# Kernel optimization log

Measured on AMD Instinct MI355X. Metric: run time of the kernel, lower is better.

## Reference

```python
import jax, jax.numpy as jnp
import numpy as np

N = 200000
NNZ = 6400000
E = 500000
IN_P, IN_F, IN_N = 62, 37, 37
HID, LAT, DEC_HID = 256, 128, 64


def _p(key, shape, scale=0.05):
    return scale * jax.random.normal(key, shape, dtype=jnp.float32)


def setup_inputs() -> dict:
    key = jax.random.key(0)
    ks = jax.random.split(key, 32)
    inp = {
        'x_process': jax.random.normal(ks[0], (N, IN_P), dtype=jnp.float32),
        'x_file': jax.random.normal(ks[1], (N, IN_F), dtype=jnp.float32),
        'x_network': jax.random.normal(ks[2], (N, IN_N), dtype=jnp.float32),
        'adj_rows': jax.random.randint(ks[3], (NNZ,), 0, N, dtype=jnp.int32),
        'adj_cols': jax.random.randint(ks[4], (NNZ,), 0, N, dtype=jnp.int32),
        'adj_vals': jax.random.uniform(ks[5], (NNZ,), dtype=jnp.float32) / 32.0,
        'edge_src': jax.random.randint(ks[6], (E,), 0, N, dtype=jnp.int32),
        'edge_dst': jax.random.randint(ks[7], (E,), 0, N, dtype=jnp.int32),
        # per-view encoder params (weights stored [in, out])
        'Wp1': _p(ks[8], (IN_P, HID)), 'bp1': jnp.zeros((HID,), jnp.float32),
        'Wp2': _p(ks[9], (HID, LAT)), 'bp2': jnp.zeros((LAT,), jnp.float32),
        'Wf1': _p(ks[10], (IN_F, HID)), 'bf1': jnp.zeros((HID,), jnp.float32),
        'Wf2': _p(ks[11], (HID, LAT)), 'bf2': jnp.zeros((LAT,), jnp.float32),
        'Wn1': _p(ks[12], (IN_N, HID)), 'bn1': jnp.zeros((HID,), jnp.float32),
        'Wn2': _p(ks[13], (HID, LAT)), 'bn2': jnp.zeros((LAT,), jnp.float32),
        # gates
        'Wgp': _p(ks[14], (LAT, 1)), 'bgp': jnp.zeros((1,), jnp.float32),
        'Wgf': _p(ks[15], (LAT, 1)), 'bgf': jnp.zeros((1,), jnp.float32),
        'Wgn': _p(ks[16], (LAT, 1)), 'bgn': jnp.zeros((1,), jnp.float32),
        # mlp edge decoder
        'Wd1': _p(ks[17], (4 * LAT, DEC_HID)), 'bd1': jnp.zeros((DEC_HID,), jnp.float32),
        'Wd2': _p(ks[18], (DEC_HID, 1)), 'bd2': jnp.zeros((1,), jnp.float32),
    }
    return inp


def _spmm(rows, cols, vals, x):
    # sparse (COO) adjacency @ dense x : gather cols, scale, scatter-add into rows
    return jax.ops.segment_sum(vals[:, None] * x[cols], rows, num_segments=N)


def _encode_view(x, rows, cols, vals, W1, b1, W2, b2):
    h = jax.nn.relu(_spmm(rows, cols, vals, x) @ W1 + b1)  # dropout=0 / eval mode
    return _spmm(rows, cols, vals, h) @ W2 + b2


def reference(x_process, x_file, x_network, adj_rows, adj_cols, adj_vals,
              edge_src, edge_dst,
              Wp1, bp1, Wp2, bp2, Wf1, bf1, Wf2, bf2, Wn1, bn1, Wn2, bn2,
              Wgp, bgp, Wgf, bgf, Wgn, bgn, Wd1, bd1, Wd2, bd2):
    zp = _encode_view(x_process, adj_rows, adj_cols, adj_vals, Wp1, bp1, Wp2, bp2)
    zf = _encode_view(x_file, adj_rows, adj_cols, adj_vals, Wf1, bf1, Wf2, bf2)
    zn = _encode_view(x_network, adj_rows, adj_cols, adj_vals, Wn1, bn1, Wn2, bn2)
    # multi-view softmax gating -> fused latent [N, LAT]
    scores = jnp.concatenate([zp @ Wgp + bgp, zf @ Wgf + bgf, zn @ Wgn + bgn], axis=1)
    alpha = jax.nn.softmax(scores, axis=1)
    z = alpha[:, 0:1] * zp + alpha[:, 1:2] * zf + alpha[:, 2:3] * zn
    # mlp edge decoder: gather src/dst, concat features, small MLP
    zs, zd = z[edge_src], z[edge_dst]
    feats = jnp.concatenate([zs, zd, zs * zd, jnp.abs(zs - zd)], axis=1)  # [E, 4*LAT]
    logits = jax.nn.relu(feats @ Wd1 + bd1) @ Wd2 + bd2
    return logits[:, 0]
```

## Files before the change

kernel.cpp:

```cpp
#include <hip/hip_runtime.h>
#include <math.h>

#define Nn 200000
#define NNZV 6400000
#define NE 500000
#define HID 256
#define LAT 128

typedef _Float16 h2 __attribute__((ext_vector_type(2)));
typedef _Float16 f16x4 __attribute__((ext_vector_type(4)));
typedef _Float16 f16x8 __attribute__((ext_vector_type(8)));
typedef float f32x4 __attribute__((ext_vector_type(4)));
typedef short s16x8 __attribute__((ext_vector_type(8)));
struct alignas(8) H4 { _Float16 h[4]; };

__global__ __launch_bounds__(256) void k_zero(int* __restrict__ cnt){
  int i = blockIdx.x*256 + threadIdx.x;
  if(i < Nn) cnt[i] = 0;
}

__global__ __launch_bounds__(256) void k_count(const int* __restrict__ rows, int* __restrict__ cnt){
  int i = blockIdx.x*256 + threadIdx.x;
  if(i < NNZV) atomicAdd(&cnt[rows[i]], 1);
}

__global__ __launch_bounds__(512) void k_scan_block(const int* __restrict__ cnt, int* __restrict__ incl, int* __restrict__ bsum){
  __shared__ int s[512];
  int t = threadIdx.x;
  int i = blockIdx.x*512 + t;
  int v = (i < Nn) ? cnt[i] : 0;
  s[t] = v; __syncthreads();
  for(int off = 1; off < 512; off <<= 1){
    int x = (t >= off) ? s[t-off] : 0;
    __syncthreads();
    s[t] += x;
    __syncthreads();
  }
  if(i < Nn) incl[i] = s[t];
  if(t == 511) bsum[blockIdx.x] = s[t];
}

__global__ __launch_bounds__(512) void k_scan_bsum(int* __restrict__ bsum, int nb){
  __shared__ int s[512];
  int t = threadIdx.x;
  int v = (t < nb) ? bsum[t] : 0;
  s[t] = v; __syncthreads();
  for(int off = 1; off < 512; off <<= 1){
    int x = (t >= off) ? s[t-off] : 0;
    __syncthreads();
    s[t] += x;
    __syncthreads();
  }
  if(t < nb) bsum[t] = s[t] - v;
}

__global__ __launch_bounds__(256) void k_finish(const int* __restrict__ incl, const int* __restrict__ boff,
                                                int* __restrict__ row_ptr, int* __restrict__ cur){
  int i = blockIdx.x*256 + threadIdx.x;
  if(i < Nn){
    int v = incl[i] + boff[i >> 9];
    row_ptr[i+1] = v;
    if(i < Nn-1) cur[i+1] = v;
  }
  if(i == 0){ row_ptr[0] = 0; cur[0] = 0; }
}

__global__ __launch_bounds__(256) void k_scatter(const int* __restrict__ rows, const int* __restrict__ cols,
    const float* __restrict__ vals, int* __restrict__ cur,
    int* __restrict__ cols_s, _Float16* __restrict__ vals_s){
  int i = blockIdx.x*256 + threadIdx.x;
  if(i >= NNZV) return;
  int r = rows[i];
  int j = atomicAdd(&cur[r], 1);
  cols_s[j] = cols[i];
  vals_s[j] = (_Float16)vals[i];
}

__global__ __launch_bounds__(256) void k_xpack(const float* __restrict__ xp, const float* __restrict__ xf,
    const float* __restrict__ xn, _Float16* __restrict__ xc0, _Float16* __restrict__ xtl){
  int idx = blockIdx.x*256 + threadIdx.x;
  int row = idx/18, c8 = idx - row*18;
  if(row >= Nn) return;
  H4 ha, hb;
  #pragma unroll
  for(int q = 0; q < 8; q++){
    int c = c8*8 + q;
    float x;
    if(c < 62)       x = xp[row*62 + c];
    else if(c < 99)  x = xf[row*37 + (c-62)];
    else if(c == 99) x = 0.f;
    else if(c < 137) x = xn[row*37 + (c-100)];
    else             x = 0.f;
    if(q < 4) ha.h[q] = (_Float16)x; else hb.h[q-4] = (_Float16)x;
  }
  if(c8 < 16){
    *(H4*)&xc0[(size_t)row*128 + c8*8]     = ha;
    *(H4*)&xc0[(size_t)row*128 + c8*8 + 4] = hb;
  } else {
    int t = (c8-16)*8;
    *(H4*)&xtl[(size_t)row*16 + t]     = ha;
    *(H4*)&xtl[(size_t)row*16 + t + 4] = hb;
  }
}

__global__ __launch_bounds__(256) void k_wpackF(
    const float* __restrict__ Wp1, const float* __restrict__ Wf1, const float* __restrict__ Wn1,
    const float* __restrict__ Wp2, const float* __restrict__ Wf2, const float* __restrict__ Wn2,
    const float* __restrict__ Wd1,
    _Float16* __restrict__ w1fp, _Float16* __restrict__ w1ff, _Float16* __restrict__ w1fn,
    _Float16* __restrict__ w2fp, _Float16* __restrict__ w2ff, _Float16* __restrict__ w2fn,
    _Float16* __restrict__ wdf){
  int i = blockIdx.x*256 + threadIdx.x;
  if(i >= 22528) return;
  f16x8 o;
  if(i >= 18432){
    int r = i - 18432;
    int w = r >> 10, kt = (r >> 8) & 3, nt = (r >> 6) & 3, l = r & 63;
    int krow = w*128 + kt*32 + (l>>4)*8, col = nt*16 + (l&15);
    #pragma unroll
    for(int j = 0; j < 8; j++)
      o[j] = (_Float16)Wd1[(krow + j)*64 + col];
    *(f16x8*)&wdf[(size_t)r*8] = o;
    return;
  }
  int v = i / 6144, rem = i - v*6144;
  const float* W1 = (v==0)?Wp1:((v==1)?Wf1:Wn1);
  const float* W2 = (v==0)?Wp2:((v==1)?Wf2:Wn2);
  _Float16* d1 = (v==0)?w1fp:((v==1)?w1ff:w1fn);
  _Float16* d2 = (v==0)?w2fp:((v==1)?w2ff:w2fn);
  int Kv = (v==0)?62:37;
  if(rem < 2048){
    int kt = rem >> 10, r2 = rem & 1023;
    int nt = r2 >> 6, l = r2 & 63;
    int krow = kt*32 + (l>>4)*8, col = nt*16 + (l&15);
    #pragma unroll
    for(int j = 0; j < 8; j++){
      int k = krow + j;
      o[j] = (k < Kv) ? (_Float16)W1[k*256 + col] : (_Float16)0.f;
    }
    *(f16x8*)&d1[rem*8] = o;
  } else {
    int r = rem - 2048;
    int kt = r >> 9, nt = (r >> 6) & 7, l = r & 63;
    int krow = kt*32 + (l>>4)*8, col = nt*16 + (l&15);
    #pragma unroll
    for(int j = 0; j < 8; j++)
      o[j] = (_Float16)W2[(krow + j)*128 + col];
    *(f16x8*)&d2[r*8] = o;
  }
}

__global__ void k_const(const float* b2p, const float* Wgp, const float* bgp,
                        const float* b2f, const float* Wgf, const float* bgf,
                        const float* b2n, const float* Wgn, const float* bgn,
                        float* c3){
  int l = threadIdx.x;
  float p = 0.f, f = 0.f, n = 0.f;
  for(int j = l; j < LAT; j += 64){
    p += b2p[j]*Wgp[j];
    f += b2f[j]*Wgf[j];
    n += b2n[j]*Wgn[j];
  }
  #pragma unroll
  for(int off = 32; off >= 1; off >>= 1){
    p += __shfl_xor(p, off);
    f += __shfl_xor(f, off);
    n += __shfl_xor(n, off);
  }
  if(l == 0){ c3[0] = p + bgp[0]; c3[1] = f + bgf[0]; c3[2] = n + bgn[0]; }
}

__device__ __forceinline__ void encode_view(
    int tid, int row0, int voff, int Kv, int vidx,
    const _Float16 (*sT)[152], _Float16 (*sTv)[72], _Float16 (*hT)[264],
    const _Float16* __restrict__ w1frag, const float* __restrict__ b1,
    const _Float16* __restrict__ w2frag,
    _Float16* __restrict__ Y3){
  int w = tid >> 6, l = tid & 63;
  int kg = l >> 4, er = l & 15;
  int mrow = (w & 1)*16 + er;

  {
    int row = tid >> 3, c0 = (tid & 7)*8;
    f16x8 vv;
    #pragma unroll
    for(int q = 0; q < 8; q++){
      int c = c0 + q;
      vv[q] = (c < Kv) ? sT[row][voff + c] : (_Float16)0.f;
    }
    *(f16x8*)&sTv[row][c0] = vv;
  }
  __syncthreads();

  {
    f16x8 a0 = *(const f16x8*)&sTv[mrow][kg*8];
    f16x8 a1 = *(const f16x8*)&sTv[mrow][32 + kg*8];
    int ntb = (w >> 1)*8;
    #pragma unroll
    for(int nt8 = 0; nt8 < 8; nt8++){
      int nt = ntb + nt8;
      f16x8 b0 = *(const f16x8*)&w1frag[(size_t)((0*16 + nt)*64 + l)*8];
      f16x8 b1v = *(const f16x8*)&w1frag[(size_t)((1*16 + nt)*64 + l)*8];
      f32x4 acc = {0.f, 0.f, 0.f, 0.f};
      acc = __builtin_amdgcn_mfma_f32_16x16x32_f16(a0, b0, acc, 0, 0, 0);
      acc = __builtin_amdgcn_mfma_f32_16x16x32_f16(a1, b1v, acc, 0, 0, 0);
      int col = nt*16 + er;
      float bb = b1[col];
      #pragma unroll
      for(int j = 0; j < 4; j++)
        hT[(w & 1)*16 + kg*4 + j][col] = (_Float16)fmaxf(acc[j] + bb, 0.f);
    }
  }
  __syncthreads();

  {
    f16x8 af[8];
    #pragma unroll
    for(int kt = 0; kt < 8; kt++)
      af[kt] = *(const f16x8*)&hT[mrow][kt*32 + kg*8];
    __syncthreads();
    _Float16* yst = &hT[0][0];
    int ntb = (w >> 1)*4;
    #pragma unroll
    for(int nt4 = 0; nt4 < 4; nt4++){
      int nt = ntb + nt4;
      f32x4 acc = {0.f, 0.f, 0.f, 0.f};
      #pragma unroll
      for(int kt = 0; kt < 8; kt++){
        f16x8 bf = *(const f16x8*)&w2frag[(size_t)((kt*8 + nt)*64 + l)*8];
        acc = __builtin_amdgcn_mfma_f32_16x16x32_f16(af[kt], bf, acc, 0, 0, 0);
      }
      int col = nt*16 + er;
      #pragma unroll
      for(int j = 0; j < 4; j++)
        yst[((w & 1)*16 + kg*4 + j)*132 + col] = (_Float16)acc[j];
    }
    __syncthreads();
    int row = tid >> 3, c0 = (tid & 7)*16;
    f16x8 y0 = *(const f16x8*)&yst[row*132 + c0];
    f16x8 y1 = *(const f16x8*)&yst[row*132 + c0 + 8];
    _Float16* yo = &Y3[(size_t)(row0 + row)*384 + vidx*128 + c0];
    *(f16x8*)yo       = y0;
    *(f16x8*)(yo + 8) = y1;
  }
  __syncthreads();
}

__global__ __launch_bounds__(256, 5) void k_encfused(
    const int* __restrict__ row_ptr, const int* __restrict__ cols_s, const _Float16* __restrict__ vals_s,
    const _Float16* __restrict__ xc0, const _Float16* __restrict__ xtl,
    const _Float16* __restrict__ w1fp, const float* __restrict__ bp1, const _Float16* __restrict__ w2fp,
    const _Float16* __restrict__ w1ff, const float* __restrict__ bf1, const _Float16* __restrict__ w2ff,
    const _Float16* __restrict__ w1fn, const float* __restrict__ bn1, const _Float16* __restrict__ w2fn,
    _Float16* __restrict__ Y3){
  __shared__ _Float16 sT[32][152];
  __shared__ _Float16 sTv[32][72];
  __shared__ _Float16 hT[32][264];
  int tid = threadIdx.x;
  int lane = tid & 63, wid = tid >> 6;
  int hl = lane & 31;
  int half = lane >> 5;
  int base = lane & 32;
  int row0 = blockIdx.x * 32;
  bool hast = (hl < 4);
  const char* xc0b = (const char*)xc0;
  const char* xtlb = (const char*)xtl;

  for(int p = 0; p < 4; p++){
    int rr = wid*8 + p*2 + half;
    int r = row0 + rr;
    int start = row_ptr[r], end = row_ptr[r+1];
    int len = end - start;
    int lenO = __shfl(len, lane ^ 32);
    int lenmax = len > lenO ? len : lenO;
    float a0 = 0.f, a1 = 0.f, a2 = 0.f, a3 = 0.f;
    float t0 = 0.f, t1 = 0.f, t2 = 0.f, t3 = 0.f;
    for(int j0 = 0; j0 < lenmax; j0 += 32){
      int m = len - j0; if(m > 32) m = 32; if(m < 0) m = 0;
      int mO = lenO - j0; if(mO > 32) mO = 32; if(mO < 0) mO = 0;
      int mmax = m > mO ? m : mO;
      int mycol = 0; float myval = 0.f;
      if(hl < m){
        mycol = cols_s[start + j0 + hl];
        myval = (float)vals_s[start + j0 + hl];
      }
      int mpad = (mmax + 3) & ~3;
      for(int k = 0; k < mpad; k += 4){
        #pragma unroll
        for(int q = 0; q < 4; q++){
          int c = __shfl(mycol, base + k + q);
          float v = __shfl(myval, base + k + q);
          f16x4 xa = *(const f16x4*)(xc0b + (((unsigned)c) << 8) + hl*8);
          a0 = fmaf((float)xa[0], v, a0);
          a1 = fmaf((float)xa[1], v, a1);
          a2 = fmaf((float)xa[2], v, a2);
          a3 = fmaf((float)xa[3], v, a3);
          if(hast){
            f16x4 xb = *(const f16x4*)(xtlb + ((unsigned)c)*32u + hl*8);
            t0 = fmaf((float)xb[0], v, t0);
            t1 = fmaf((float)xb[1], v, t1);
            t2 = fmaf((float)xb[2], v, t2);
            t3 = fmaf((float)xb[3], v, t3);
          }
        }
      }
    }
    h2 s01; s01[0] = (_Float16)a0; s01[1] = (_Float16)a1;
    h2 s23; s23[0] = (_Float16)a2; s23[1] = (_Float16)a3;
    *(h2*)&sT[rr][4*hl]     = s01;
    *(h2*)&sT[rr][4*hl + 2] = s23;
    if(hast){
      h2 u01; u01[0] = (_Float16)t0; u01[1] = (_Float16)t1;
      h2 u23; u23[0] = (_Float16)t2; u23[1] = (_Float16)t3;
      *(h2*)&sT[rr][128 + 4*hl]     = u01;
      *(h2*)&sT[rr][128 + 4*hl + 2] = u23;
    }
  }
  __syncthreads();

  encode_view(tid, row0, 0,   62, 0, sT, sTv, hT, w1fp, bp1, w2fp, Y3);
  encode_view(tid, row0, 62,  37, 1, sT, sTv, hT, w1ff, bf1, w2ff, Y3);
  encode_view(tid, row0, 100, 37, 2, sT, sTv, hT, w1fn, bn1, w2fn, Y3);
}

__global__ __launch_bounds__(256, 8) void k_spmm2f(
    const int* __restrict__ row_ptr, const int* __restrict__ cols_s, const _Float16* __restrict__ vals_s,
    const _Float16* __restrict__ Y3,
    const float* __restrict__ Wgp, const float* __restrict__ Wgf, const float* __restrict__ Wgn,
    const float* __restrict__ c3,
    const float* __restrict__ b2p, const float* __restrict__ b2f, const float* __restrict__ b2n,
    _Float16* __restrict__ z){
  int tid = threadIdx.x;
  int lane = tid & 63;
  int hl = lane & 31;
  int half = lane >> 5;
  int base = lane & 32;
  int r = blockIdx.x*8 + (tid >> 6)*2 + half;
  int start = row_ptr[r], end = row_ptr[r+1];
  int len = end - start;
  int lenO = __shfl(len, lane ^ 32);
  int lenmax = len > lenO ? len : lenO;
  unsigned lo = hl*8;
  float ap0=0.f, ap1=0.f, ap2=0.f, ap3=0.f;
  float af0=0.f, af1=0.f, af2=0.f, af3=0.f;
  float an0=0.f, an1=0.f, an2=0.f, an3=0.f;
  const char* Yb = (const char*)Y3;
  for(int j0 = 0; j0 < lenmax; j0 += 32){
    int m = len - j0; if(m > 32) m = 32; if(m < 0) m = 0;
    int mO = lenO - j0; if(mO > 32) mO = 32; if(mO < 0) mO = 0;
    int mmax = m > mO ? m : mO;
    int mycol = 0; float myval = 0.f;
    if(hl < m){
      mycol = cols_s[start + j0 + hl];
      myval = (float)vals_s[start + j0 + hl];
    }
    int mpad = (mmax + 3) & ~3;
    for(int k = 0; k < mpad; k += 4){
      #pragma unroll
      for(int q = 0; q < 4; q++){
        int c = __shfl(mycol, base + k + q);
        float v = __shfl(myval, base + k + q);
        const char* p = Yb + ((unsigned)c)*768u + lo;
        f16x4 yp = *(const f16x4*)(p);
        f16x4 yf = *(const f16x4*)(p + 256);
        f16x4 yn = *(const f16x4*)(p + 512);
        ap0 = fmaf((float)yp[0], v, ap0); ap1 = fmaf((float)yp[1], v, ap1);
        ap2 = fmaf((float)yp[2], v, ap2); ap3 = fmaf((float)yp[3], v, ap3);
        af0 = fmaf((float)yf[0], v, af0); af1 = fmaf((float)yf[1], v, af1);
        af2 = fmaf((float)yf[2], v, af2); af3 = fmaf((float)yf[3], v, af3);
        an0 = fmaf((float)yn[0], v, an0); an1 = fmaf((float)yn[1], v, an1);
        an2 = fmaf((float)yn[2], v, an2); an3 = fmaf((float)yn[3], v, an3);
      }
    }
  }
  int o = hl*4;
  float4 wp = *(const float4*)&Wgp[o];
  float4 wf = *(const float4*)&Wgf[o];
  float4 wn = *(const float4*)&Wgn[o];
  float scp = ap0*wp.x + ap1*wp.y + ap2*wp.z + ap3*wp.w;
  float scf = af0*wf.x + af1*wf.y + af2*wf.z + af3*wf.w;
  float scn = an0*wn.x + an1*wn.y + an2*wn.z + an3*wn.w;
  #pragma unroll
  for(int off = 16; off >= 1; off >>= 1){
    scp += __shfl_xor(scp, off);
    scf += __shfl_xor(scf, off);
    scn += __shfl_xor(scn, off);
  }
  float sp = scp + c3[0], sf = scf + c3[1], sn = scn + c3[2];
  float mx = fmaxf(sp, fmaxf(sf, sn));
  float ep = expf(sp - mx), ef = expf(sf - mx), en = expf(sn - mx);
  float inv = 1.f / (ep + ef + en);
  float A0 = ep*inv, A1 = ef*inv, A2 = en*inv;
  float4 bp = *(const float4*)&b2p[o];
  float4 bf = *(const float4*)&b2f[o];
  float4 bn = *(const float4*)&b2n[o];
  H4 uz;
  uz.h[0] = (_Float16)(A0*(ap0 + bp.x) + A1*(af0 + bf.x) + A2*(an0 + bn.x));
  uz.h[1] = (_Float16)(A0*(ap1 + bp.y) + A1*(af1 + bf.y) + A2*(an1 + bn.y));
  uz.h[2] = (_Float16)(A0*(ap2 + bp.z) + A1*(af2 + bf.z) + A2*(an2 + bn.z));
  uz.h[3] = (_Float16)(A0*(ap3 + bp.w) + A1*(af3 + bf.w) + A2*(an3 + bn.w));
  *(H4*)&z[(size_t)r*LAT + o] = uz;
}

#define DEC_TILES (NE/16)
__global__ __launch_bounds__(256) void k_dec(
    const _Float16* __restrict__ z, const int* __restrict__ esrc, const int* __restrict__ edst,
    const _Float16* __restrict__ wdf, const float* __restrict__ bd1,
    const float* __restrict__ Wd2, const float* __restrict__ bd2, float* __restrict__ out){
  __shared__ float part[4][16][68];
  int tid = threadIdx.x;
  int w  = tid >> 6;
  int l  = tid & 63;
  int erow = l & 15;
  int kg   = l >> 4;
  const f16x8* wb = (const f16x8*)wdf + (size_t)w*1024 + l;

  int n0 = (tid & 15) * 4;
  int e2 = tid >> 4;
  float4 bb1 = *(const float4*)&bd1[n0];
  float4 w2v = *(const float4*)&Wd2[n0];
  float bias2 = bd2[0];

  for(int tile = blockIdx.x; tile < DEC_TILES; tile += gridDim.x){
    int e = tile*16 + erow;
    int si = esrc[e], di = edst[e];
    const f16x8* zs = (const f16x8*)&z[(size_t)si*LAT];
    const f16x8* zd = (const f16x8*)&z[(size_t)di*LAT];
    f16x8 afr[4];
    if(w == 0){
      #pragma unroll
      for(int kt = 0; kt < 4; kt++) afr[kt] = zs[kt*4 + kg];
    } else if(w == 1){
      #pragma unroll
      for(int kt = 0; kt < 4; kt++) afr[kt] = zd[kt*4 + kg];
    } else if(w == 2){
      #pragma unroll
      for(int kt = 0; kt < 4; kt++) afr[kt] = zs[kt*4 + kg] * zd[kt*4 + kg];
    } else {
      #pragma unroll
      for(int kt = 0; kt < 4; kt++){
        f16x8 d = zs[kt*4 + kg] - zd[kt*4 + kg];
        s16x8 m = __builtin_bit_cast(s16x8, d) & (short)0x7fff;
        afr[kt] = __builtin_bit_cast(f16x8, m);
      }
    }
    f32x4 zero = {0.f, 0.f, 0.f, 0.f};
    f32x4 acc[4] = {zero, zero, zero, zero};
    #pragma unroll
    for(int kt = 0; kt < 4; kt++){
      #pragma unroll
      for(int nt = 0; nt < 4; nt++){
        f16x8 bf = wb[kt*256 + nt*64];
        acc[nt] = __builtin_amdgcn_mfma_f32_16x16x32_f16(afr[kt], bf, acc[nt], 0, 0, 0);
      }
    }
    #pragma unroll
    for(int nt = 0; nt < 4; nt++){
      #pragma unroll
      for(int j = 0; j < 4; j++)
        part[w][kg*4 + j][nt*16 + erow] = acc[nt][j];
    }
    __syncthreads();
    float s0 = part[0][e2][n0+0] + part[1][e2][n0+0] + part[2][e2][n0+0] + part[3][e2][n0+0];
    float s1 = part[0][e2][n0+1] + part[1][e2][n0+1] + part[2][e2][n0+1] + part[3][e2][n0+1];
    float s2 = part[0][e2][n0+2] + part[1][e2][n0+2] + part[2][e2][n0+2] + part[3][e2][n0+2];
    float s3 = part[0][e2][n0+3] + part[1][e2][n0+3] + part[2][e2][n0+3] + part[3][e2][n0+3];
    float p = fmaxf(s0 + bb1.x, 0.f)*w2v.x + fmaxf(s1 + bb1.y, 0.f)*w2v.y
            + fmaxf(s2 + bb1.z, 0.f)*w2v.z + fmaxf(s3 + bb1.w, 0.f)*w2v.w;
    #pragma unroll
    for(int off = 1; off < 16; off <<= 1) p += __shfl_xor(p, off);
    if((tid & 15) == 0) out[tile*16 + e2] = p + bias2;
    __syncthreads();
  }
}

extern "C" void kernel_launch(void* const* d_in, const int* in_sizes, int n_in,
                              void* d_out, int out_size, void* d_ws, size_t ws_size,
                              hipStream_t stream) {
  const float* xp  = (const float*)d_in[0];
  const float* xf  = (const float*)d_in[1];
  const float* xn  = (const float*)d_in[2];
  const int* arows = (const int*)d_in[3];
  const int* acols = (const int*)d_in[4];
  const float* avals = (const float*)d_in[5];
  const int* esrc  = (const int*)d_in[6];
  const int* edst  = (const int*)d_in[7];
  const float* Wp1 = (const float*)d_in[8];  const float* bp1 = (const float*)d_in[9];
  const float* Wp2 = (const float*)d_in[10]; const float* bp2 = (const float*)d_in[11];
  const float* Wf1 = (const float*)d_in[12]; const float* bf1 = (const float*)d_in[13];
  const float* Wf2 = (const float*)d_in[14]; const float* bf2w = (const float*)d_in[15];
  const float* Wn1 = (const float*)d_in[16]; const float* bn1 = (const float*)d_in[17];
  const float* Wn2 = (const float*)d_in[18]; const float* bn2 = (const float*)d_in[19];
  const float* Wgp = (const float*)d_in[20]; const float* bgp = (const float*)d_in[21];
  const float* Wgf = (const float*)d_in[22]; const float* bgf = (const float*)d_in[23];
  const float* Wgn = (const float*)d_in[24]; const float* bgn = (const float*)d_in[25];
  const float* Wd1 = (const float*)d_in[26]; const float* bd1 = (const float*)d_in[27];
  const float* Wd2 = (const float*)d_in[28]; const float* bd2 = (const float*)d_in[29];
  float* out = (float*)d_out;
  (void)in_sizes; (void)n_in; (void)out_size; (void)ws_size;

  char* base = (char*)d_ws;
  size_t off = 0;
  auto alloc = [&](size_t nbytes) -> char* {
    off = (off + 255) & ~(size_t)255;
    char* p = base + off;
    off += nbytes;
    return p;
  };
  int*      row_ptr = (int*)     alloc((size_t)(Nn + 1) * 4);
  int*      cols_s  = (int*)     alloc((size_t)NNZV * 4);
  _Float16* vals_s  = (_Float16*)alloc((size_t)NNZV * 2);
  _Float16* xcat0   = (_Float16*)alloc((size_t)Nn * 128 * 2);
  _Float16* xtail   = (_Float16*)alloc((size_t)Nn * 16 * 2);
  _Float16* Y3      = (_Float16*)alloc((size_t)Nn * 384 * 2);
  float*    c3      = (float*)   alloc(256);
  _Float16* w1fp = (_Float16*)alloc(16384*2);
  _Float16* w1ff = (_Float16*)alloc(16384*2);
  _Float16* w1fn = (_Float16*)alloc(16384*2);
  _Float16* w2fp = (_Float16*)alloc(32768*2);
  _Float16* w2ff = (_Float16*)alloc(32768*2);
  _Float16* w2fn = (_Float16*)alloc(32768*2);
  _Float16* wdf  = (_Float16*)alloc(32768*2);
  _Float16* z = xcat0;
  int* cur  = (int*)((char*)xcat0);
  int* incl = (int*)((char*)xcat0 + 1000000);
  int* bsum = (int*)((char*)xcat0 + 2000000);

  int NB = (Nn + 511) / 512;

  k_zero   <<<(Nn + 255)/256, 256, 0, stream>>>(cur);
  k_count  <<<(NNZV + 255)/256, 256, 0, stream>>>(arows, cur);
  k_scan_block<<<NB, 512, 0, stream>>>(cur, incl, bsum);
  k_scan_bsum<<<1, 512, 0, stream>>>(bsum, NB);
  k_finish <<<(Nn + 255)/256, 256, 0, stream>>>(incl, bsum, row_ptr, cur);
  k_scatter<<<(NNZV + 255)/256, 256, 0, stream>>>(arows, acols, avals, cur, cols_s, vals_s);

  k_xpack<<<(Nn*18 + 255)/256, 256, 0, stream>>>(xp, xf, xn, xcat0, xtail);
  k_wpackF<<<(22528 + 255)/256, 256, 0, stream>>>(Wp1, Wf1, Wn1, Wp2, Wf2, Wn2, Wd1,
                                                  w1fp, w1ff, w1fn, w2fp, w2ff, w2fn, wdf);
  k_const<<<1, 64, 0, stream>>>(bp2, Wgp, bgp, bf2w, Wgf, bgf, bn2, Wgn, bgn, c3);

  k_encfused<<<Nn/32, 256, 0, stream>>>(row_ptr, cols_s, vals_s, xcat0, xtail,
      w1fp, bp1, w2fp,  w1ff, bf1, w2ff,  w1fn, bn1, w2fn,
      Y3);

  k_spmm2f<<<Nn/8, 256, 0, stream>>>(row_ptr, cols_s, vals_s, Y3,
      Wgp, Wgf, Wgn, c3, bp2, bf2w, bn2, z);

  k_dec<<<2048, 256, 0, stream>>>(z, esrc, edst, wdf, bd1, Wd2, bd2, out);
}
```

Baseline: 2.099 ms.

## Split fused encoder into separate SpMM and MLP kernels via global buffer

The fused first-layer kernel is split in two. A new SpMM kernel with higher occupancy writes the aggregated features into the Y3 buffer, padded per view to 64 columns. A separate MLP kernel then reads those rows in place and overwrites Y3 with the per-view outputs. This removes the occupancy limit the MFMA and shared-memory stages imposed on the latency-bound gather. The cost is an extra zero-fill pass over Y3, an extra global round trip of about 150MB, and two more launches.

After: 2.142 ms. 1.02x slower.

```diff
diff --git a/kernel.cpp b/kernel.cpp
--- a/kernel.cpp
+++ b/kernel.cpp
@@ -74,6 +74,13 @@
   int j = atomicAdd(&cur[r], 1);
   cols_s[j] = cols[i];
   vals_s[j] = (_Float16)vals[i];
+}
+
+__global__ __launch_bounds__(256) void k_zf(float4* __restrict__ p, int n){
+  int i = blockIdx.x*256 + threadIdx.x;
+  int stride = gridDim.x*256;
+  float4 z = make_float4(0.f,0.f,0.f,0.f);
+  for(; i < n; i += stride) p[i] = z;
 }
 
 __global__ __launch_bounds__(256) void k_xpack(const float* __restrict__ xp, const float* __restrict__ xf,
@@ -170,31 +177,88 @@
   if(l == 0){ c3[0] = p + bgp[0]; c3[1] = f + bgf[0]; c3[2] = n + bgn[0]; }
 }
 
-__device__ __forceinline__ void encode_view(
-    int tid, int row0, int voff, int Kv, int vidx,
-    const _Float16 (*sT)[152], _Float16 (*sTv)[72], _Float16 (*hT)[264],
+__global__ __launch_bounds__(256, 8) void k_spmm1(
+    const int* __restrict__ row_ptr, const int* __restrict__ cols_s, const _Float16* __restrict__ vals_s,
+    const _Float16* __restrict__ xc0, const _Float16* __restrict__ xtl,
+    _Float16* __restrict__ sG){
+  int tid = threadIdx.x;
+  int lane = tid & 63;
+  int hl = lane & 31;
+  int half = lane >> 5;
+  int base = lane & 32;
+  int r = blockIdx.x*8 + (tid >> 6)*2 + half;
+  int start = row_ptr[r], end = row_ptr[r+1];
+  int len = end - start;
+  int lenO = __shfl(len, lane ^ 32);
+  int lenmax = len > lenO ? len : lenO;
+  bool hast = (hl < 4);
+  const char* xc0b = (const char*)xc0;
+  const char* xtlb = (const char*)xtl;
+  float a0 = 0.f, a1 = 0.f, a2 = 0.f, a3 = 0.f;
+  float t0 = 0.f, t1 = 0.f, t2 = 0.f, t3 = 0.f;
+  for(int j0 = 0; j0 < lenmax; j0 += 32){
+    int m = len - j0; if(m > 32) m = 32; if(m < 0) m = 0;
+    int mO = lenO - j0; if(mO > 32) mO = 32; if(mO < 0) mO = 0;
+    int mmax = m > mO ? m : mO;
+    int mycol = 0; float myval = 0.f;
+    if(hl < m){
+      mycol = cols_s[start + j0 + hl];
+      myval = (float)vals_s[start + j0 + hl];
+    }
+    int mpad = (mmax + 3) & ~3;
+    for(int k = 0; k < mpad; k += 4){
+      #pragma unroll
+      for(int q = 0; q < 4; q++){
+        int c = __shfl(mycol, base + k + q);
+        float v = __shfl(myval, base + k + q);
+        f16x4 xa = *(const f16x4*)(xc0b + (((unsigned)c) << 8) + hl*8);
+        a0 = fmaf((float)xa[0], v, a0);
+        a1 = fmaf((float)xa[1], v, a1);
+        a2 = fmaf((float)xa[2], v, a2);
+        a3 = fmaf((float)xa[3], v, a3);
+        if(hast){
+          f16x4 xb = *(const f16x4*)(xtlb + ((unsigned)c)*32u + hl*8);
+          t0 = fmaf((float)xb[0], v, t0);
+          t1 = fmaf((float)xb[1], v, t1);
+          t2 = fmaf((float)xb[2], v, t2);
+          t3 = fmaf((float)xb[3], v, t3);
+        }
+      }
+    }
+  }
+  _Float16* row_out = sG + (size_t)r*384;
+  h2 u01; u01[0] = (_Float16)a0; u01[1] = (_Float16)a1;
+  h2 u23; u23[0] = (_Float16)a2; u23[1] = (_Float16)a3;
+  int c0 = 4*hl;
+  if(hl == 15){
+    *(h2*)&row_out[60] = u01;
+    *(h2*)&row_out[64] = u23;
+  } else {
+    int sbase = (c0 < 62) ? c0 : ((c0 < 100) ? c0 + 2 : c0 + 28);
+    *(h2*)&row_out[sbase]     = u01;
+    *(h2*)&row_out[sbase + 2] = u23;
+  }
+  if(hast){
+    int tb = 156 + 4*hl;
+    h2 v01; v01[0] = (_Float16)t0; v01[1] = (_Float16)t1;
+    h2 v23; v23[0] = (_Float16)t2; v23[1] = (_Float16)t3;
+    *(h2*)&row_out[tb]     = v01;
+    *(h2*)&row_out[tb + 2] = v23;
+  }
+}
+
+__device__ __forceinline__ void mlp_view(
+    int tid, int row0, int vidx,
+    f16x8 a0, f16x8 a1,
+    _Float16 (*hT)[264],
     const _Float16* __restrict__ w1frag, const float* __restrict__ b1,
     const _Float16* __restrict__ w2frag,
-    _Float16* __restrict__ Y3){
+    _Float16* Y3){
   int w = tid >> 6, l = tid & 63;
   int kg = l >> 4, er = l & 15;
   int mrow = (w & 1)*16 + er;
 
   {
-    int row = tid >> 3, c0 = (tid & 7)*8;
-    f16x8 vv;
-    #pragma unroll
-    for(int q = 0; q < 8; q++){
-      int c = c0 + q;
-      vv[q] = (c < Kv) ? sT[row][voff + c] : (_Float16)0.f;
-    }
-    *(f16x8*)&sTv[row][c0] = vv;
-  }
-  __syncthreads();
-
-  {
-    f16x8 a0 = *(const f16x8*)&sTv[mrow][kg*8];
-    f16x8 a1 = *(const f16x8*)&sTv[mrow][32 + kg*8];
     int ntb = (w >> 1)*8;
     #pragma unroll
     for(int nt8 = 0; nt8 < 8; nt8++){
@@ -246,81 +310,27 @@
   __syncthreads();
 }
 
-__global__ __launch_bounds__(256, 5) void k_encfused(
-    const int* __restrict__ row_ptr, const int* __restrict__ cols_s, const _Float16* __restrict__ vals_s,
-    const _Float16* __restrict__ xc0, const _Float16* __restrict__ xtl,
+__global__ __launch_bounds__(256, 6) void k_mlp(
+    _Float16* Y3,
     const _Float16* __restrict__ w1fp, const float* __restrict__ bp1, const _Float16* __restrict__ w2fp,
     const _Float16* __restrict__ w1ff, const float* __restrict__ bf1, const _Float16* __restrict__ w2ff,
-    const _Float16* __restrict__ w1fn, const float* __restrict__ bn1, const _Float16* __restrict__ w2fn,
-    _Float16* __restrict__ Y3){
-  __shared__ _Float16 sT[32][152];
-  __shared__ _Float16 sTv[32][72];
+    const _Float16* __restrict__ w1fn, const float* __restrict__ bn1, const _Float16* __restrict__ w2fn){
   __shared__ _Float16 hT[32][264];
   int tid = threadIdx.x;
-  int lane = tid & 63, wid = tid >> 6;
-  int hl = lane & 31;
-  int half = lane >> 5;
-  int base = lane & 32;
+  int w = tid >> 6, l = tid & 63;
+  int kg = l >> 4, er = l & 15;
+  int mrow = (w & 1)*16 + er;
   int row0 = blockIdx.x * 32;
-  bool hast = (hl < 4);
-  const char* xc0b = (const char*)xc0;
-  const char* xtlb = (const char*)xtl;
-
-  for(int p = 0; p < 4; p++){
-    int rr = wid*8 + p*2 + half;
-    int r = row0 + rr;
-    int start = row_ptr[r], end = row_ptr[r+1];
-    int len = end - start;
-    int lenO = __shfl(len, lane ^ 32);
-    int lenmax = len > lenO ? len : lenO;
-    float a0 = 0.f, a1 = 0.f, a2 = 0.f, a3 = 0.f;
-    float t0 = 0.f, t1 = 0.f, t2 = 0.f, t3 = 0.f;
-    for(int j0 = 0; j0 < lenmax; j0 += 32){
-      int m = len - j0; if(m > 32) m = 32; if(m < 0) m = 0;
-      int mO = lenO - j0; if(mO > 32) mO = 32; if(mO < 0) mO = 0;
-      int mmax = m > mO ? m : mO;
-      int mycol = 0; float myval = 0.f;
-      if(hl < m){
-        mycol = cols_s[start + j0 + hl];
-        myval = (float)vals_s[start + j0 + hl];
-      }
-      int mpad = (mmax + 3) & ~3;
-      for(int k = 0; k < mpad; k += 4){
-        #pragma unroll
-        for(int q = 0; q < 4; q++){
-          int c = __shfl(mycol, base + k + q);
-          float v = __shfl(myval, base + k + q);
-          f16x4 xa = *(const f16x4*)(xc0b + (((unsigned)c) << 8) + hl*8);
-          a0 = fmaf((float)xa[0], v, a0);
-          a1 = fmaf((float)xa[1], v, a1);
-          a2 = fmaf((float)xa[2], v, a2);
-          a3 = fmaf((float)xa[3], v, a3);
-          if(hast){
-            f16x4 xb = *(const f16x4*)(xtlb + ((unsigned)c)*32u + hl*8);
-            t0 = fmaf((float)xb[0], v, t0);
-            t1 = fmaf((float)xb[1], v, t1);
-            t2 = fmaf((float)xb[2], v, t2);
-            t3 = fmaf((float)xb[3], v, t3);
-          }
-        }
-      }
-    }
-    h2 s01; s01[0] = (_Float16)a0; s01[1] = (_Float16)a1;
-    h2 s23; s23[0] = (_Float16)a2; s23[1] = (_Float16)a3;
-    *(h2*)&sT[rr][4*hl]     = s01;
-    *(h2*)&sT[rr][4*hl + 2] = s23;
-    if(hast){
-      h2 u01; u01[0] = (_Float16)t0; u01[1] = (_Float16)t1;
-      h2 u23; u23[0] = (_Float16)t2; u23[1] = (_Float16)t3;
-      *(h2*)&sT[rr][128 + 4*hl]     = u01;
-      *(h2*)&sT[rr][128 + 4*hl + 2] = u23;
-    }
-  }
+
+  const f16x8* sgr = (const f16x8*)(Y3 + (size_t)(row0 + mrow)*384);
+  f16x8 a00 = sgr[0*8 + kg], a01 = sgr[0*8 + kg + 4];
+  f16x8 a10 = sgr[1*8 + kg], a11 = sgr[1*8 + kg + 4];
+  f16x8 a20 = sgr[2*8 + kg], a21 = sgr[2*8 + kg + 4];
   __syncthreads();
 
-  encode_view(tid, row0, 0,   62, 0, sT, sTv, hT, w1fp, bp1, w2fp, Y3);
-  encode_view(tid, row0, 62,  37, 1, sT, sTv, hT, w1ff, bf1, w2ff, Y3);
-  encode_view(tid, row0, 100, 37, 2, sT, sTv, hT, w1fn, bn1, w2fn, Y3);
+  mlp_view(tid, row0, 0, a00, a01, hT, w1fp, bp1, w2fp, Y3);
+  mlp_view(tid, row0, 1, a10, a11, hT, w1ff, bf1, w2ff, Y3);
+  mlp_view(tid, row0, 2, a20, a21, hT, w1fn, bn1, w2fn, Y3);
 }
 
 __global__ __launch_bounds__(256, 8) void k_spmm2f(
@@ -510,9 +520,6 @@
   int*      row_ptr = (int*)     alloc((size_t)(Nn + 1) * 4);
   int*      cols_s  = (int*)     alloc((size_t)NNZV * 4);
   _Float16* vals_s  = (_Float16*)alloc((size_t)NNZV * 2);
-  _Float16* xcat0   = (_Float16*)alloc((size_t)Nn * 128 * 2);
-  _Float16* xtail   = (_Float16*)alloc((size_t)Nn * 16 * 2);
-  _Float16* Y3      = (_Float16*)alloc((size_t)Nn * 384 * 2);
   float*    c3      = (float*)   alloc(256);
   _Float16* w1fp = (_Float16*)alloc(16384*2);
   _Float16* w1ff = (_Float16*)alloc(16384*2);
@@ -521,10 +528,13 @@
   _Float16* w2ff = (_Float16*)alloc(32768*2);
   _Float16* w2fn = (_Float16*)alloc(32768*2);
   _Float16* wdf  = (_Float16*)alloc(32768*2);
+  _Float16* Y3   = (_Float16*)alloc((size_t)Nn * 384 * 2);
+  _Float16* xcat0= (_Float16*)alloc((size_t)Nn * 128 * 2);
+  _Float16* xtail= (_Float16*)alloc((size_t)Nn * 16 * 2);
   _Float16* z = xcat0;
-  int* cur  = (int*)((char*)xcat0);
-  int* incl = (int*)((char*)xcat0 + 1000000);
-  int* bsum = (int*)((char*)xcat0 + 2000000);
+  int* cur  = (int*)((char*)Y3);
+  int* incl = (int*)((char*)Y3 + 1000000);
+  int* bsum = (int*)((char*)Y3 + 2000000);
 
   int NB = (Nn + 511) / 512;
 
@@ -540,9 +550,12 @@
                                                   w1fp, w1ff, w1fn, w2fp, w2ff, w2fn, wdf);
   k_const<<<1, 64, 0, stream>>>(bp2, Wgp, bgp, bf2w, Wgf, bgf, bn2, Wgn, bgn, c3);
 
-  k_encfused<<<Nn/32, 256, 0, stream>>>(row_ptr, cols_s, vals_s, xcat0, xtail,
-      w1fp, bp1, w2fp,  w1ff, bf1, w2ff,  w1fn, bn1, w2fn,
-      Y3);
+  k_zf<<<2048, 256, 0, stream>>>((float4*)Y3, Nn*48);
+
+  k_spmm1<<<Nn/8, 256, 0, stream>>>(row_ptr, cols_s, vals_s, xcat0, xtail, Y3);
+
+  k_mlp<<<Nn/32, 256, 0, stream>>>(Y3,
+      w1fp, bp1, w2fp,  w1ff, bf1, w2ff,  w1fn, bn1, w2fn);
 
   k_spmm2f<<<Nn/8, 256, 0, stream>>>(row_ptr, cols_s, vals_s, Y3,
       Wgp, Wgf, Wgn, c3, bp2, bf2w, bn2, z);
```
